# Kernel tuning notes

Measured on AMD Instinct MI355X. Metric: run time of the kernel, lower is better.

The kernel has to match this reference:

```python
import jax, jax.numpy as jnp
import numpy as np

EMB, CLS, M_MARGIN, B = 512, 20000, 4, 256
LAMB = 1500.0 / 1.1          # AngleLoss lambda at it=1: max(5, 1500/(1+0.1*1))
LMD_INTER = 0.01
PI = 3.14159265              # constant used in original sphereface code


def setup_inputs() -> dict:
    key = jax.random.key(0)
    k1, k2, k3 = jax.random.split(key, 3)
    emb = jax.random.normal(k1, (B, EMB), dtype=jnp.float32)
    y = jax.random.randint(k2, (B,), 0, CLS)
    # weight initialized uniform(-1,1) then column-renormalized inside forward
    W = jax.random.uniform(k3, (EMB, CLS), dtype=jnp.float32, minval=-1.0, maxval=1.0)
    return {"emb": emb, "y": y, "W": W}


def _forward(emb, W, y):
    b = emb.shape[0]
    # --- ASoftmax (sphereface AngleLinear, m=4, phiflag=True) ---
    nm_W = W / jnp.linalg.norm(W, axis=0, keepdims=True)            # unit columns [E,C]
    xlen = jnp.linalg.norm(emb, axis=1, keepdims=True)              # [B,1]
    cos = jnp.clip((emb @ nm_W) / xlen, -1.0, 1.0)                  # [B,C]
    cos_m = 8.0 * cos**4 - 8.0 * cos**2 + 1.0                        # cos(4*theta)
    theta = jnp.arccos(jax.lax.stop_gradient(cos))                   # torch: acos on .data
    k = jnp.floor(M_MARGIN * theta / PI)
    sign = 1.0 - 2.0 * jnp.mod(k, 2.0)                               # (-1)^k
    phi = sign * cos_m - 2.0 * k
    cos_s = cos * xlen                                               # logits[0]
    phi_s = phi * xlen
    # --- AngleLoss (gamma=0) ---
    f = 1.0 / (1.0 + LAMB)
    onehot = jax.nn.one_hot(y, CLS, dtype=cos_s.dtype)               # [B,C]
    output = cos_s + onehot * f * (phi_s - cos_s)
    logpt = jax.nn.log_softmax(output, axis=1)
    logpt_t = jnp.take_along_axis(logpt, y[:, None], axis=1)[:, 0]
    ce = -jnp.mean(logpt_t)
    # --- MHE inter-class loss: sum_{i, j != y_i} 1/||w_{y_i} - w_j||^2 ---
    # unit columns => ||w_a - w_b||^2 = 2 - 2 <w_a, w_b>; avoids the
    # [E, B*C] scatter/repeat intermediate of the original.
    ws = nm_W[:, y]                                                  # [E,B]
    cosWW = ws.T @ nm_W                                              # [B,C]
    dist2 = jnp.maximum(2.0 - 2.0 * cosWW, 0.0)
    mask = onehot > 0.5                                              # j == y_i (z_n == 0)
    inv = jnp.where(mask, 0.0, 1.0 / jnp.where(mask, 1.0, dist2))
    inter = jnp.sum(inv) / (b * (CLS - 1))
    loss = ce + LMD_INTER * inter
    return loss, cos_s, inter


def reference(emb, y, W):
    loss, logits0, inter = _forward(emb, W, y)
    pred = jnp.argmax(logits0, axis=1)
    acc = jnp.mean((pred == y).astype(jnp.float32))
    return loss, logits0, acc, inter
```

## Files before the change

kernel.cpp:

```cpp
#include <hip/hip_runtime.h>
#include <hip/hip_bf16.h>
#include <math.h>

#define B_N   256
#define EMB_N 512
#define CLS_N 20000
#define NMB   157
#define PI_F  3.14159265f
#define F_CONST ((float)(1.1 / 1501.1))

typedef __bf16 bf16x8 __attribute__((ext_vector_type(8)));
typedef float  f32x4  __attribute__((ext_vector_type(4)));
typedef unsigned short u16x8 __attribute__((ext_vector_type(8)));

__device__ __forceinline__ unsigned short f2bf(float f) {
    unsigned u = __float_as_uint(f);
    unsigned r = (u + 0x7FFFu + ((u >> 16) & 1u)) >> 16;
    return (unsigned short)r;
}

__device__ __forceinline__ void merge4(float& M, float& S, float& VM, int& VI,
                                       float m2, float s2, float vm2, int vi2) {
    float mn = fmaxf(M, m2);
    if (mn == -INFINITY) { S = 0.f; }
    else S = S * __expf(M - mn) + s2 * __expf(m2 - mn);
    M = mn;
    if (vm2 > VM || (vm2 == VM && vi2 < VI)) { VM = vm2; VI = vi2; }
}

__global__ __launch_bounds__(256) void prep_kernel(
    const float* __restrict__ emb, const int* __restrict__ y,
    const float* __restrict__ W,
    unsigned short* __restrict__ Abf,
    float* __restrict__ xlen_a, float* __restrict__ inv_xlen_a,
    float* __restrict__ inv_wny_a, float* __restrict__ mod_val_a,
    float* __restrict__ accums)
{
    const int b = blockIdx.x;
    const int t = threadIdx.x;
    if (b == 0 && t < 4) accums[t] = 0.f;
    const int yb = y[b];
    const float* erow = emb + (size_t)b * EMB_N;
    float se = 0.f, sw = 0.f, dt = 0.f;
    for (int e = t; e < EMB_N; e += 256) {
        float ev = erow[e];
        float wv = W[(size_t)e * CLS_N + yb];
        Abf[(size_t)b * EMB_N + e]         = f2bf(ev);
        Abf[(size_t)(B_N + b) * EMB_N + e] = f2bf(wv);
        se += ev * ev; sw += wv * wv; dt += ev * wv;
    }
    __shared__ float r0[256], r1[256], r2[256];
    r0[t] = se; r1[t] = sw; r2[t] = dt;
    __syncthreads();
    for (int s = 128; s > 0; s >>= 1) {
        if (t < s) { r0[t] += r0[t + s]; r1[t] += r1[t + s]; r2[t] += r2[t + s]; }
        __syncthreads();
    }
    if (t == 0) {
        float xlen = sqrtf(r0[0]);
        float wn   = sqrtf(r1[0]);
        float inv_x = 1.f / xlen;
        float inv_w = 1.f / wn;
        float cos_t = r2[0] * inv_w * inv_x;
        cos_t = fminf(1.f, fmaxf(-1.f, cos_t));
        float c2 = cos_t * cos_t;
        float cos_m = 8.f * c2 * c2 - 8.f * c2 + 1.f;
        float theta = acosf(cos_t);
        float k = floorf(4.f * theta / PI_F);
        float sgn = 1.f - 2.f * fmodf(k, 2.f);
        float phi = sgn * cos_m - 2.f * k;
        float cos_s = cos_t * xlen;
        float phi_s = phi * xlen;
        xlen_a[b] = xlen;
        inv_xlen_a[b] = inv_x;
        inv_wny_a[b] = inv_w;
        mod_val_a[b] = cos_s + F_CONST * (phi_s - cos_s);
    }
}

__global__ __launch_bounds__(256, 3) void mfma_gemm_kernel(
    const float* __restrict__ W, const unsigned short* __restrict__ Abf,
    const int* __restrict__ y,
    const float* __restrict__ xlen_a, const float* __restrict__ inv_xlen_a,
    const float* __restrict__ inv_wny_a,
    float* __restrict__ logits, float4* __restrict__ partials,
    float* __restrict__ inter_sum)
{
    __shared__ alignas(16) char smem[53248];
    float*  sSq   = (float*)smem;
    float*  sIwc  = (float*)(smem + 2048);
    float4* sPart = (float4*)(smem + 2560);
    float*  red   = (float*)(smem + 6656);

    const int orig = blockIdx.x;
    const int xcd  = orig & 7;
    const int wgid = (xcd < 4 ? xcd * 79 : 316 + (xcd - 4) * 78) + (orig >> 3);
    const int tile  = wgid >> 2;
    const int slice = wgid & 3;
    const int m0    = tile * 128;
    const int gn0   = slice * 128;

    const int t    = threadIdx.x;
    const int lane = t & 63;
    const int wid  = t >> 6;
    const int wr   = wid >> 1;
    const int wc   = wid & 1;
    const int r16  = lane & 15;
    const int kh   = lane >> 4;

    const char* Bb = (const char*)Abf;

    f32x4 acc[4][4] = {};
    float2 aq[2][8];
    float ssq0 = 0.f, ssq1 = 0.f;

    const int c2 = (t & 63) * 2;
    const int ko = t >> 6;
    const int gc = min(m0 + c2, CLS_N - 2);

    const int srow = lane >> 2;
    const int srcq = (lane & 3) ^ ((lane >> 2) & 3);

    #define ISSUE_A(kt, s)                                                        \
        { _Pragma("unroll")                                                       \
          for (int p = 0; p < 8; ++p)                                             \
              aq[s][p] = *reinterpret_cast<const float2*>(                        \
                  &W[(size_t)((kt) + ko * 8 + p) * CLS_N + gc]);                  \
        }

    #define ISSUE_B(kt, slab)                                                     \
        { _Pragma("unroll")                                                       \
          for (int i = 0; i < 2; ++i) {                                           \
              int slot = wid * 2 + i;                                             \
              int row  = slot * 16 + srow;                                        \
              __builtin_amdgcn_global_load_lds(                                   \
                  (const __attribute__((address_space(1))) unsigned int*)         \
                      (Bb + (size_t)(gn0 + row) * 1024 + (size_t)(kt) * 2         \
                          + srcq * 16),                                           \
                  (__attribute__((address_space(3))) unsigned int*)               \
                      (smem + 20480 + (slab) * 8192 + slot * 1024),               \
                  16, 0, 0);                                                      \
          } }

    #define WRITE_A(s, buf)                                                       \
        { u16x8 u0, u1; float s0 = 0.f, s1 = 0.f;                                 \
          _Pragma("unroll")                                                       \
          for (int p = 0; p < 8; ++p) {                                           \
              float vx = aq[s][p].x, vy = aq[s][p].y;                             \
              u0[p] = f2bf(vx); u1[p] = f2bf(vy);                                 \
              s0 += vx * vx; s1 += vy * vy;                                       \
          }                                                                       \
          ssq0 += s0; ssq1 += s1;                                                 \
          *reinterpret_cast<u16x8*>(smem + (buf) * 10240 + c2 * 80 + ko * 16) = u0; \
          *reinterpret_cast<u16x8*>(smem + (buf) * 10240 + (c2 + 1) * 80 + ko * 16) = u1; }

    #define COMPUTE(buf, slab)                                                    \
        { bf16x8 af[4], bfr[4];                                                   \
          _Pragma("unroll")                                                       \
          for (int mi = 0; mi < 4; ++mi) {                                        \
              int row = wr * 64 + mi * 16 + r16;                                  \
              af[mi] = *reinterpret_cast<const bf16x8*>(                          \
                  smem + (buf) * 10240 + row * 80 + kh * 16);                     \
          }                                                                       \
          _Pragma("unroll")                                                       \
          for (int ni = 0; ni < 4; ++ni) {                                        \
              int rowb = wc * 64 + ni * 16 + r16;                                 \
              bfr[ni] = *reinterpret_cast<const bf16x8*>(                         \
                  smem + 20480 + (slab) * 8192 + rowb * 64                        \
                  + ((kh ^ (rowb & 3)) << 4));                                    \
          }                                                                       \
          __builtin_amdgcn_s_setprio(1);                                          \
          _Pragma("unroll")                                                       \
          for (int mi = 0; mi < 4; ++mi)                                          \
              _Pragma("unroll")                                                   \
              for (int ni = 0; ni < 4; ++ni)                                      \
                  acc[mi][ni] = __builtin_amdgcn_mfma_f32_16x16x32_bf16(          \
                      af[mi], bfr[ni], acc[mi][ni], 0, 0, 0);                     \
          __builtin_amdgcn_s_setprio(0); }

    #define FENCE() __builtin_amdgcn_sched_barrier(0);

    ISSUE_A(0, 0)  ISSUE_B(0, 0)

    #pragma unroll
    for (int tt = 0; tt < 16; ++tt) {
        WRITE_A(tt & 1, tt & 1)
        if (tt < 15) {
            ISSUE_A((tt + 1) * 32, (tt + 1) & 1)
            ISSUE_B((tt + 1) * 32, (tt + 1) & 3)
            FENCE()
            asm volatile("s_waitcnt vmcnt(10) lgkmcnt(0)" ::: "memory");
        } else {
            FENCE()
            asm volatile("s_waitcnt vmcnt(0) lgkmcnt(0)" ::: "memory");
        }
        FENCE()
        asm volatile("s_barrier" ::: "memory");
        FENCE()
        COMPUTE(tt & 1, tt & 3)
        FENCE()
    }
    #undef ISSUE_A
    #undef ISSUE_B
    #undef WRITE_A
    #undef COMPUTE
    #undef FENCE

    __syncthreads();

    sSq[ko * 128 + c2]     = ssq0;
    sSq[ko * 128 + c2 + 1] = ssq1;
    __syncthreads();
    if (t < 128) {
        float s = sSq[t] + sSq[128 + t] + sSq[256 + t] + sSq[384 + t];
        sIwc[t] = rsqrtf(s);
    }
    __syncthreads();

    float iwc[4][4];
    #pragma unroll
    for (int mi = 0; mi < 4; ++mi)
        #pragma unroll
        for (int r = 0; r < 4; ++r)
            iwc[mi][r] = sIwc[wr * 64 + mi * 16 + kh * 4 + r];

    if (slice < 2) {
        #pragma unroll
        for (int ni = 0; ni < 4; ++ni) {
            int bl = wc * 64 + ni * 16 + r16;
            int b  = gn0 + bl;
            float xl  = xlen_a[b];
            float ixl = inv_xlen_a[b];
            float M = -INFINITY, S = 0.f, VM = -INFINITY; int VI = 0x7fffffff;
            #pragma unroll
            for (int mi = 0; mi < 4; ++mi) {
                int cb = m0 + wr * 64 + mi * 16 + kh * 4;
                if (cb < CLS_N) {
                    f32x4 vout;
                    #pragma unroll
                    for (int r = 0; r < 4; ++r) {
                        float cosv = acc[mi][ni][r] * iwc[mi][r] * ixl;
                        cosv = fminf(1.f, fmaxf(-1.f, cosv));
                        float v = cosv * xl;
                        vout[r] = v;
                        if (v > M) { S = S * __expf(M - v) + 1.f; M = v; }
                        else       { S += __expf(v - M); }
                        if (v > VM) { VM = v; VI = cb + r; }
                    }
                    *reinterpret_cast<f32x4*>(&logits[(size_t)b * CLS_N + cb]) = vout;
                }
            }
            #pragma unroll
            for (int d = 16; d < 64; d <<= 1) {
                float m2  = __shfl_xor(M, d);
                float s2  = __shfl_xor(S, d);
                float vm2 = __shfl_xor(VM, d);
                int   vi2 = __shfl_xor(VI, d);
                merge4(M, S, VM, VI, m2, s2, vm2, vi2);
            }
            if (kh == 0) sPart[bl * 2 + wr] = make_float4(M, S, VM, __int_as_float(VI));
        }
        __syncthreads();
        if (t < 128) {
            float4 p0 = sPart[t * 2 + 0], p1 = sPart[t * 2 + 1];
            float M = p0.x, S = p0.y, VM = p0.z; int VI = __float_as_int(p0.w);
            merge4(M, S, VM, VI, p1.x, p1.y, p1.z, __float_as_int(p1.w));
            partials[(size_t)(gn0 + t) * NMB + tile] =
                make_float4(M, S, VM, __int_as_float(VI));
        }
    } else {
        float part = 0.f;
        #pragma unroll
        for (int ni = 0; ni < 4; ++ni) {
            int b = (slice - 2) * 128 + wc * 64 + ni * 16 + r16;
            float iwy = inv_wny_a[b];
            int   yb  = y[b];
            #pragma unroll
            for (int mi = 0; mi < 4; ++mi) {
                int cb = m0 + wr * 64 + mi * 16 + kh * 4;
                #pragma unroll
                for (int r = 0; r < 4; ++r) {
                    int c = cb + r;
                    if (c < CLS_N && c != yb) {
                        float cww = acc[mi][ni][r] * iwc[mi][r] * iwy;
                        float d2 = fmaxf(2.f - 2.f * cww, 0.f);
                        part += 1.f / d2;
                    }
                }
            }
        }
        red[t] = part;
        __syncthreads();
        for (int s = 128; s > 0; s >>= 1) {
            if (t < s) red[t] += red[t + s];
            __syncthreads();
        }
        if (t == 0) atomicAdd(inter_sum, red[0]);
    }
}

__global__ __launch_bounds__(64) void reduce_kernel(
    const float4* __restrict__ partials, const float* __restrict__ logits,
    const int* __restrict__ y, const float* __restrict__ mod_val_a,
    float* __restrict__ accums, float* __restrict__ out)
{
    const int b = blockIdx.x;
    const int t = threadIdx.x;
    float M = -INFINITY, S = 0.f, VM = -INFINITY; int VI = 0x7fffffff;
    for (int i = t; i < NMB; i += 64) {
        float4 p = partials[(size_t)b * NMB + i];
        merge4(M, S, VM, VI, p.x, p.y, p.z, __float_as_int(p.w));
    }
    #pragma unroll
    for (int d = 1; d < 64; d <<= 1) {
        float m2  = __shfl_xor(M, d);
        float s2  = __shfl_xor(S, d);
        float vm2 = __shfl_xor(VM, d);
        int   vi2 = __shfl_xor(VI, d);
        merge4(M, S, VM, VI, m2, s2, vm2, vi2);
    }
    if (t == 0) {
        int   yb  = y[b];
        float vyb = logits[(size_t)b * CLS_N + yb];
        float mv  = mod_val_a[b];
        float m2 = fmaxf(M, mv);
        float s2 = S * __expf(M - m2) - __expf(vyb - m2) + __expf(mv - m2);
        float lse = m2 + logf(s2);
        atomicAdd(&accums[0], -(mv - lse));
        if (VI == yb) atomicAdd(&accums[1], 1.f);
        __threadfence();
        int old = atomicAdd((int*)&accums[3], 1);
        if (old == B_N - 1) {
            float ce    = atomicAdd(&accums[0], 0.f) / (float)B_N;
            float acc   = atomicAdd(&accums[1], 0.f) / (float)B_N;
            float inter = atomicAdd(&accums[2], 0.f) / (float)((double)B_N * (CLS_N - 1));
            out[0] = ce + 0.01f * inter;
            out[(size_t)1 + (size_t)B_N * CLS_N + 0] = acc;
            out[(size_t)1 + (size_t)B_N * CLS_N + 1] = inter;
        }
    }
}

extern "C" void kernel_launch(void* const* d_in, const int* in_sizes, int n_in,
                              void* d_out, int out_size, void* d_ws, size_t ws_size,
                              hipStream_t stream) {
    const float* emb = (const float*)d_in[0];
    const int*   y   = (const int*)d_in[1];
    const float* W   = (const float*)d_in[2];
    float* out = (float*)d_out;
    float* logits = out + 1;

    const size_t ABF_OFF  = 0;
    const size_t PART_OFF = 524288;
    const size_t SC_OFF   = PART_OFF + (size_t)B_N * NMB * 16;

    unsigned short* Abf = (unsigned short*)((char*)d_ws + ABF_OFF);
    float4* partials   = (float4*)((char*)d_ws + PART_OFF);
    float*  xlen_a     = (float*)((char*)d_ws + SC_OFF);
    float*  inv_xlen_a = xlen_a + 256;
    float*  inv_wny_a  = xlen_a + 512;
    float*  mod_val_a  = xlen_a + 768;
    float*  accums     = xlen_a + 1024;

    prep_kernel<<<B_N, 256, 0, stream>>>(emb, y, W, Abf,
                                         xlen_a, inv_xlen_a, inv_wny_a, mod_val_a,
                                         accums);
    mfma_gemm_kernel<<<628, 256, 0, stream>>>(W, Abf, y,
                                              xlen_a, inv_xlen_a, inv_wny_a,
                                              logits, partials, accums + 2);
    reduce_kernel<<<B_N, 64, 0, stream>>>(partials, logits, y, mod_val_a,
                                          accums, out);
}
```

Measured before the change: 53.85 us.

## Split GEMM block work across eight waves with 512 threads

The GEMM kernel goes from 256 to 512 threads per block. Each wave now computes a 64x32 output sub-tile instead of 64x64, and the A staging and B async loads are spread over eight waves, so each thread issues fewer loads. Scratch-memory offsets, the sum-of-squares reduction, the wait counts and the tree reduction are all resized to match. The aim is more waves in flight to hide memory latency, at the cost of less register-level reuse per wave and tighter register limits from the new launch bounds.

```diff
diff --git a/kernel.cpp b/kernel.cpp
--- a/kernel.cpp
+++ b/kernel.cpp
@@ -11,7 +11,7 @@
 
 typedef __bf16 bf16x8 __attribute__((ext_vector_type(8)));
 typedef float  f32x4  __attribute__((ext_vector_type(4)));
-typedef unsigned short u16x8 __attribute__((ext_vector_type(8)));
+typedef unsigned short u16x4 __attribute__((ext_vector_type(4)));
 
 __device__ __forceinline__ unsigned short f2bf(float f) {
     unsigned u = __float_as_uint(f);
@@ -78,7 +78,7 @@
     }
 }
 
-__global__ __launch_bounds__(256, 3) void mfma_gemm_kernel(
+__global__ __launch_bounds__(512, 4) void mfma_gemm_kernel(
     const float* __restrict__ W, const unsigned short* __restrict__ Abf,
     const int* __restrict__ y,
     const float* __restrict__ xlen_a, const float* __restrict__ inv_xlen_a,
@@ -88,9 +88,9 @@
 {
     __shared__ alignas(16) char smem[53248];
     float*  sSq   = (float*)smem;
-    float*  sIwc  = (float*)(smem + 2048);
-    float4* sPart = (float4*)(smem + 2560);
-    float*  red   = (float*)(smem + 6656);
+    float*  sIwc  = (float*)(smem + 4096);
+    float4* sPart = (float4*)(smem + 4608);
+    float*  red   = (float*)(smem + 8704);
 
     const int orig = blockIdx.x;
     const int xcd  = orig & 7;
@@ -103,15 +103,15 @@
     const int t    = threadIdx.x;
     const int lane = t & 63;
     const int wid  = t >> 6;
-    const int wr   = wid >> 1;
-    const int wc   = wid & 1;
+    const int wr   = wid >> 2;
+    const int wq   = wid & 3;
     const int r16  = lane & 15;
     const int kh   = lane >> 4;
 
     const char* Bb = (const char*)Abf;
 
-    f32x4 acc[4][4] = {};
-    float2 aq[2][8];
+    f32x4 acc[4][2] = {};
+    float2 aq[2][4];
     float ssq0 = 0.f, ssq1 = 0.f;
 
     const int c2 = (t & 63) * 2;
@@ -123,39 +123,35 @@
 
     #define ISSUE_A(kt, s)                                                        \
         { _Pragma("unroll")                                                       \
-          for (int p = 0; p < 8; ++p)                                             \
+          for (int p = 0; p < 4; ++p)                                             \
               aq[s][p] = *reinterpret_cast<const float2*>(                        \
-                  &W[(size_t)((kt) + ko * 8 + p) * CLS_N + gc]);                  \
+                  &W[(size_t)((kt) + ko * 4 + p) * CLS_N + gc]);                  \
         }
 
     #define ISSUE_B(kt, slab)                                                     \
-        { _Pragma("unroll")                                                       \
-          for (int i = 0; i < 2; ++i) {                                           \
-              int slot = wid * 2 + i;                                             \
-              int row  = slot * 16 + srow;                                        \
-              __builtin_amdgcn_global_load_lds(                                   \
-                  (const __attribute__((address_space(1))) unsigned int*)         \
-                      (Bb + (size_t)(gn0 + row) * 1024 + (size_t)(kt) * 2         \
-                          + srcq * 16),                                           \
-                  (__attribute__((address_space(3))) unsigned int*)               \
-                      (smem + 20480 + (slab) * 8192 + slot * 1024),               \
-                  16, 0, 0);                                                      \
-          } }
+        { int row = wid * 16 + srow;                                              \
+          __builtin_amdgcn_global_load_lds(                                       \
+              (const __attribute__((address_space(1))) unsigned int*)             \
+                  (Bb + (size_t)(gn0 + row) * 1024 + (size_t)(kt) * 2             \
+                      + srcq * 16),                                               \
+              (__attribute__((address_space(3))) unsigned int*)                   \
+                  (smem + 20480 + (slab) * 8192 + wid * 1024),                    \
+              16, 0, 0); }
 
     #define WRITE_A(s, buf)                                                       \
-        { u16x8 u0, u1; float s0 = 0.f, s1 = 0.f;                                 \
+        { u16x4 u0, u1; float s0 = 0.f, s1 = 0.f;                                 \
           _Pragma("unroll")                                                       \
-          for (int p = 0; p < 8; ++p) {                                           \
+          for (int p = 0; p < 4; ++p) {                                           \
               float vx = aq[s][p].x, vy = aq[s][p].y;                             \
               u0[p] = f2bf(vx); u1[p] = f2bf(vy);                                 \
               s0 += vx * vx; s1 += vy * vy;                                       \
           }                                                                       \
           ssq0 += s0; ssq1 += s1;                                                 \
-          *reinterpret_cast<u16x8*>(smem + (buf) * 10240 + c2 * 80 + ko * 16) = u0; \
-          *reinterpret_cast<u16x8*>(smem + (buf) * 10240 + (c2 + 1) * 80 + ko * 16) = u1; }
+          *reinterpret_cast<u16x4*>(smem + (buf) * 10240 + c2 * 80 + ko * 8) = u0; \
+          *reinterpret_cast<u16x4*>(smem + (buf) * 10240 + (c2 + 1) * 80 + ko * 8) = u1; }
 
     #define COMPUTE(buf, slab)                                                    \
-        { bf16x8 af[4], bfr[4];                                                   \
+        { bf16x8 af[4], bfr[2];                                                   \
           _Pragma("unroll")                                                       \
           for (int mi = 0; mi < 4; ++mi) {                                        \
               int row = wr * 64 + mi * 16 + r16;                                  \
@@ -163,8 +159,8 @@
                   smem + (buf) * 10240 + row * 80 + kh * 16);                     \
           }                                                                       \
           _Pragma("unroll")                                                       \
-          for (int ni = 0; ni < 4; ++ni) {                                        \
-              int rowb = wc * 64 + ni * 16 + r16;                                 \
+          for (int ni = 0; ni < 2; ++ni) {                                        \
+              int rowb = wq * 32 + ni * 16 + r16;                                 \
               bfr[ni] = *reinterpret_cast<const bf16x8*>(                         \
                   smem + 20480 + (slab) * 8192 + rowb * 64                        \
                   + ((kh ^ (rowb & 3)) << 4));                                    \
@@ -173,7 +169,7 @@
           _Pragma("unroll")                                                       \
           for (int mi = 0; mi < 4; ++mi)                                          \
               _Pragma("unroll")                                                   \
-              for (int ni = 0; ni < 4; ++ni)                                      \
+              for (int ni = 0; ni < 2; ++ni)                                      \
                   acc[mi][ni] = __builtin_amdgcn_mfma_f32_16x16x32_bf16(          \
                       af[mi], bfr[ni], acc[mi][ni], 0, 0, 0);                     \
           __builtin_amdgcn_s_setprio(0); }
@@ -189,7 +185,7 @@
             ISSUE_A((tt + 1) * 32, (tt + 1) & 1)
             ISSUE_B((tt + 1) * 32, (tt + 1) & 3)
             FENCE()
-            asm volatile("s_waitcnt vmcnt(10) lgkmcnt(0)" ::: "memory");
+            asm volatile("s_waitcnt vmcnt(5) lgkmcnt(0)" ::: "memory");
         } else {
             FENCE()
             asm volatile("s_waitcnt vmcnt(0) lgkmcnt(0)" ::: "memory");
@@ -212,7 +208,9 @@
     sSq[ko * 128 + c2 + 1] = ssq1;
     __syncthreads();
     if (t < 128) {
-        float s = sSq[t] + sSq[128 + t] + sSq[256 + t] + sSq[384 + t];
+        float s = 0.f;
+        #pragma unroll
+        for (int g = 0; g < 8; ++g) s += sSq[g * 128 + t];
         sIwc[t] = rsqrtf(s);
     }
     __syncthreads();
@@ -226,8 +224,8 @@
 
     if (slice < 2) {
         #pragma unroll
-        for (int ni = 0; ni < 4; ++ni) {
-            int bl = wc * 64 + ni * 16 + r16;
+        for (int ni = 0; ni < 2; ++ni) {
+            int bl = wq * 32 + ni * 16 + r16;
             int b  = gn0 + bl;
             float xl  = xlen_a[b];
             float ixl = inv_xlen_a[b];
@@ -271,8 +269,8 @@
     } else {
         float part = 0.f;
         #pragma unroll
-        for (int ni = 0; ni < 4; ++ni) {
-            int b = (slice - 2) * 128 + wc * 64 + ni * 16 + r16;
+        for (int ni = 0; ni < 2; ++ni) {
+            int b = (slice - 2) * 128 + wq * 32 + ni * 16 + r16;
             float iwy = inv_wny_a[b];
             int   yb  = y[b];
             #pragma unroll
@@ -291,7 +289,7 @@
         }
         red[t] = part;
         __syncthreads();
-        for (int s = 128; s > 0; s >>= 1) {
+        for (int s = 256; s > 0; s >>= 1) {
             if (t < s) red[t] += red[t + s];
             __syncthreads();
         }
@@ -365,7 +363,7 @@
     prep_kernel<<<B_N, 256, 0, stream>>>(emb, y, W, Abf,
                                          xlen_a, inv_xlen_a, inv_wny_a, mod_val_a,
                                          accums);
-    mfma_gemm_kernel<<<628, 256, 0, stream>>>(W, Abf, y,
+    mfma_gemm_kernel<<<628, 512, 0, stream>>>(W, Abf, y,
                                               xlen_a, inv_xlen_a, inv_wny_a,
                                               logits, partials, accums + 2);
     reduce_kernel<<<B_N, 64, 0, stream>>>(partials, logits, y, mod_val_a,
```

After: 54.18 us. About the same (+0.6%).

## Widen GEMM workgroups to 512 threads covering 256 columns per tile

Applied to the files above, without the earlier changes.

Each workgroup now uses 8 waves and covers a 128x256 output tile instead of 128x128, halving the grid to 314 blocks. The fp32 W tile is loaded and converted to bf16 once per 256 B-columns instead of twice, which cuts the redundant W reads and conversion work. B staging drops from four slabs to double buffering, and a second barrier is added after compute to protect buffer reuse. The trade-off is lower occupancy per CU, an extra barrier per k-step and fewer blocks than CUs to balance.

```diff
diff --git a/kernel.cpp b/kernel.cpp
--- a/kernel.cpp
+++ b/kernel.cpp
@@ -11,7 +11,7 @@
 
 typedef __bf16 bf16x8 __attribute__((ext_vector_type(8)));
 typedef float  f32x4  __attribute__((ext_vector_type(4)));
-typedef unsigned short u16x8 __attribute__((ext_vector_type(8)));
+typedef unsigned short u16x4 __attribute__((ext_vector_type(4)));
 
 __device__ __forceinline__ unsigned short f2bf(float f) {
     unsigned u = __float_as_uint(f);
@@ -26,6 +26,11 @@
     else S = S * __expf(M - mn) + s2 * __expf(m2 - mn);
     M = mn;
     if (vm2 > VM || (vm2 == VM && vi2 < VI)) { VM = vm2; VI = vi2; }
+}
+
+__device__ __forceinline__ int map314(int orig) {
+    int xcd = orig & 7;
+    return (xcd < 2 ? xcd * 40 : 80 + (xcd - 2) * 39) + (orig >> 3);
 }
 
 __global__ __launch_bounds__(256) void prep_kernel(
@@ -78,7 +83,7 @@
     }
 }
 
-__global__ __launch_bounds__(256, 3) void mfma_gemm_kernel(
+__global__ __launch_bounds__(512, 2) void mfma_gemm_kernel(
     const float* __restrict__ W, const unsigned short* __restrict__ Abf,
     const int* __restrict__ y,
     const float* __restrict__ xlen_a, const float* __restrict__ inv_xlen_a,
@@ -88,30 +93,28 @@
 {
     __shared__ alignas(16) char smem[53248];
     float*  sSq   = (float*)smem;
-    float*  sIwc  = (float*)(smem + 2048);
-    float4* sPart = (float4*)(smem + 2560);
-    float*  red   = (float*)(smem + 6656);
-
-    const int orig = blockIdx.x;
-    const int xcd  = orig & 7;
-    const int wgid = (xcd < 4 ? xcd * 79 : 316 + (xcd - 4) * 78) + (orig >> 3);
-    const int tile  = wgid >> 2;
-    const int slice = wgid & 3;
+    float*  sIwc  = (float*)(smem + 4096);
+    float4* sPart = (float4*)(smem + 4608);
+    float*  red   = (float*)(smem + 12800);
+
+    const int wgid = map314(blockIdx.x);
+    const int tile  = wgid >> 1;
+    const int slice = wgid & 1;
     const int m0    = tile * 128;
-    const int gn0   = slice * 128;
+    const int gn0   = slice * 256;
 
     const int t    = threadIdx.x;
     const int lane = t & 63;
     const int wid  = t >> 6;
-    const int wr   = wid >> 1;
-    const int wc   = wid & 1;
+    const int wr   = wid >> 2;
+    const int wb   = wid & 3;
     const int r16  = lane & 15;
     const int kh   = lane >> 4;
 
     const char* Bb = (const char*)Abf;
 
     f32x4 acc[4][4] = {};
-    float2 aq[2][8];
+    float2 aq[2][4];
     float ssq0 = 0.f, ssq1 = 0.f;
 
     const int c2 = (t & 63) * 2;
@@ -123,12 +126,12 @@
 
     #define ISSUE_A(kt, s)                                                        \
         { _Pragma("unroll")                                                       \
-          for (int p = 0; p < 8; ++p)                                             \
+          for (int p = 0; p < 4; ++p)                                             \
               aq[s][p] = *reinterpret_cast<const float2*>(                        \
-                  &W[(size_t)((kt) + ko * 8 + p) * CLS_N + gc]);                  \
-        }
-
-    #define ISSUE_B(kt, slab)                                                     \
+                  &W[(size_t)((kt) + ko * 4 + p) * CLS_N + gc]);                  \
+        }
+
+    #define ISSUE_B(kt, buf)                                                      \
         { _Pragma("unroll")                                                       \
           for (int i = 0; i < 2; ++i) {                                           \
               int slot = wid * 2 + i;                                             \
@@ -138,23 +141,23 @@
                       (Bb + (size_t)(gn0 + row) * 1024 + (size_t)(kt) * 2         \
                           + srcq * 16),                                           \
                   (__attribute__((address_space(3))) unsigned int*)               \
-                      (smem + 20480 + (slab) * 8192 + slot * 1024),               \
+                      (smem + 20480 + (buf) * 16384 + slot * 1024),               \
                   16, 0, 0);                                                      \
           } }
 
     #define WRITE_A(s, buf)                                                       \
-        { u16x8 u0, u1; float s0 = 0.f, s1 = 0.f;                                 \
+        { u16x4 u0, u1; float s0 = 0.f, s1 = 0.f;                                 \
           _Pragma("unroll")                                                       \
-          for (int p = 0; p < 8; ++p) {                                           \
+          for (int p = 0; p < 4; ++p) {                                           \
               float vx = aq[s][p].x, vy = aq[s][p].y;                             \
               u0[p] = f2bf(vx); u1[p] = f2bf(vy);                                 \
               s0 += vx * vx; s1 += vy * vy;                                       \
           }                                                                       \
           ssq0 += s0; ssq1 += s1;                                                 \
-          *reinterpret_cast<u16x8*>(smem + (buf) * 10240 + c2 * 80 + ko * 16) = u0; \
-          *reinterpret_cast<u16x8*>(smem + (buf) * 10240 + (c2 + 1) * 80 + ko * 16) = u1; }
-
-    #define COMPUTE(buf, slab)                                                    \
+          *reinterpret_cast<u16x4*>(smem + (buf) * 10240 + c2 * 80 + ko * 8) = u0; \
+          *reinterpret_cast<u16x4*>(smem + (buf) * 10240 + (c2 + 1) * 80 + ko * 8) = u1; }
+
+    #define COMPUTE(buf)                                                          \
         { bf16x8 af[4], bfr[4];                                                   \
           _Pragma("unroll")                                                       \
           for (int mi = 0; mi < 4; ++mi) {                                        \
@@ -164,9 +167,9 @@
           }                                                                       \
           _Pragma("unroll")                                                       \
           for (int ni = 0; ni < 4; ++ni) {                                        \
-              int rowb = wc * 64 + ni * 16 + r16;                                 \
+              int rowb = wb * 64 + ni * 16 + r16;                                 \
               bfr[ni] = *reinterpret_cast<const bf16x8*>(                         \
-                  smem + 20480 + (slab) * 8192 + rowb * 64                        \
+                  smem + 20480 + (buf) * 16384 + rowb * 64                        \
                   + ((kh ^ (rowb & 3)) << 4));                                    \
           }                                                                       \
           __builtin_amdgcn_s_setprio(1);                                          \
@@ -187,9 +190,9 @@
         WRITE_A(tt & 1, tt & 1)
         if (tt < 15) {
             ISSUE_A((tt + 1) * 32, (tt + 1) & 1)
-            ISSUE_B((tt + 1) * 32, (tt + 1) & 3)
+            ISSUE_B((tt + 1) * 32, (tt + 1) & 1)
             FENCE()
-            asm volatile("s_waitcnt vmcnt(10) lgkmcnt(0)" ::: "memory");
+            asm volatile("s_waitcnt vmcnt(6) lgkmcnt(0)" ::: "memory");
         } else {
             FENCE()
             asm volatile("s_waitcnt vmcnt(0) lgkmcnt(0)" ::: "memory");
@@ -197,7 +200,9 @@
         FENCE()
         asm volatile("s_barrier" ::: "memory");
         FENCE()
-        COMPUTE(tt & 1, tt & 3)
+        COMPUTE(tt & 1)
+        FENCE()
+        asm volatile("s_barrier" ::: "memory");
         FENCE()
     }
     #undef ISSUE_A
@@ -212,7 +217,9 @@
     sSq[ko * 128 + c2 + 1] = ssq1;
     __syncthreads();
     if (t < 128) {
-        float s = sSq[t] + sSq[128 + t] + sSq[256 + t] + sSq[384 + t];
+        float s = 0.f;
+        #pragma unroll
+        for (int g = 0; g < 8; ++g) s += sSq[g * 128 + t];
         sIwc[t] = rsqrtf(s);
     }
     __syncthreads();
@@ -224,11 +231,10 @@
         for (int r = 0; r < 4; ++r)
             iwc[mi][r] = sIwc[wr * 64 + mi * 16 + kh * 4 + r];
 
-    if (slice < 2) {
+    if (slice == 0) {
         #pragma unroll
         for (int ni = 0; ni < 4; ++ni) {
-            int bl = wc * 64 + ni * 16 + r16;
-            int b  = gn0 + bl;
+            int b = wb * 64 + ni * 16 + r16;
             float xl  = xlen_a[b];
             float ixl = inv_xlen_a[b];
             float M = -INFINITY, S = 0.f, VM = -INFINITY; int VI = 0x7fffffff;
@@ -258,21 +264,21 @@
                 int   vi2 = __shfl_xor(VI, d);
                 merge4(M, S, VM, VI, m2, s2, vm2, vi2);
             }
-            if (kh == 0) sPart[bl * 2 + wr] = make_float4(M, S, VM, __int_as_float(VI));
+            if (kh == 0) sPart[b * 2 + wr] = make_float4(M, S, VM, __int_as_float(VI));
         }
         __syncthreads();
-        if (t < 128) {
+        if (t < 256) {
             float4 p0 = sPart[t * 2 + 0], p1 = sPart[t * 2 + 1];
             float M = p0.x, S = p0.y, VM = p0.z; int VI = __float_as_int(p0.w);
             merge4(M, S, VM, VI, p1.x, p1.y, p1.z, __float_as_int(p1.w));
-            partials[(size_t)(gn0 + t) * NMB + tile] =
+            partials[(size_t)t * NMB + tile] =
                 make_float4(M, S, VM, __int_as_float(VI));
         }
     } else {
         float part = 0.f;
         #pragma unroll
         for (int ni = 0; ni < 4; ++ni) {
-            int b = (slice - 2) * 128 + wc * 64 + ni * 16 + r16;
+            int b = wb * 64 + ni * 16 + r16;
             float iwy = inv_wny_a[b];
             int   yb  = y[b];
             #pragma unroll
@@ -291,7 +297,7 @@
         }
         red[t] = part;
         __syncthreads();
-        for (int s = 128; s > 0; s >>= 1) {
+        for (int s = 256; s > 0; s >>= 1) {
             if (t < s) red[t] += red[t + s];
             __syncthreads();
         }
@@ -365,7 +371,7 @@
     prep_kernel<<<B_N, 256, 0, stream>>>(emb, y, W, Abf,
                                          xlen_a, inv_xlen_a, inv_wny_a, mod_val_a,
                                          accums);
-    mfma_gemm_kernel<<<628, 256, 0, stream>>>(W, Abf, y,
+    mfma_gemm_kernel<<<314, 512, 0, stream>>>(W, Abf, y,
                                               xlen_a, inv_xlen_a, inv_wny_a,
                                               logits, partials, accums + 2);
     reduce_kernel<<<B_N, 64, 0, stream>>>(partials, logits, y, mod_val_a,
```

Measured after the change: 65.47 us. 21.6% more time.
